# Kernel tuning notes

Hardware: AMD Instinct MI355X
Metric: run time of the kernel (lower is better)

## Reference

```python
import jax, jax.numpy as jnp
import numpy as np

N = 4096       # number of graph nodes
F_IN = 512     # in_features == out_features (residual connection requires it)
H = 8          # n_heads


def setup_inputs() -> dict:
    key = jax.random.key(0)
    k1, k2, k3, k4, k5 = jax.random.split(key, 5)
    s = 1.0 / np.sqrt(F_IN)  # keep projections well-scaled
    x = jax.random.normal(k1, (N, F_IN), dtype=jnp.float32)
    Wq = jax.random.normal(k2, (F_IN, F_IN), dtype=jnp.float32) * s
    Wk = jax.random.normal(k3, (F_IN, F_IN), dtype=jnp.float32) * s
    Wv = jax.random.normal(k4, (F_IN, F_IN), dtype=jnp.float32) * s
    adj = jax.random.randint(k5, (H, N, N), 0, 2, dtype=jnp.int32)
    return {"x": x, "Wq": Wq, "Wk": Wk, "Wv": Wv, "adj": adj}


def reference(x, Wq, Wk, Wv, adj):
    # Faithful to torch GraphAttentionLayer.forward (eval mode, dropout off).
    # NOTE: the torch code builds keys = input.repeat(N,1,1).detach() -> the
    # K/V inputs are stop-gradient copies of x; projections are per-node, so
    # we compute them once instead of materializing the redundant [N,N,F].
    n, f = x.shape
    d = f // H  # head dim (chunk_size)
    xk = jax.lax.stop_gradient(x)
    # nn.Linear: y = x @ W.T ; split feature dim into heads -> [H, N, d]
    Q = (x @ Wq.T).reshape(n, H, d).transpose(1, 0, 2)
    K = (xk @ Wk.T).reshape(n, H, d).transpose(1, 0, 2)
    V = (xk @ Wv.T).reshape(n, H, d).transpose(1, 0, 2)
    # scaled by sqrt(in_features) (NOT head dim), as in the original
    scores = jnp.einsum('hnd,hmd->hnm', Q, K) / jnp.sqrt(jnp.float32(f))
    scores = jnp.where(adj > 0, scores, jnp.float32(-9e15))
    attn = jax.nn.softmax(scores, axis=-1)          # [H, N, N]
    out = jnp.einsum('hnm,hmd->hnd', attn, V)       # [H, N, d]
    out = out.transpose(1, 0, 2).reshape(n, f)      # concat heads -> [N, F]
    return jax.nn.elu(out + x)[:, None, :]          # [N, 1, F] like torch
```

## Files before the change

### kernel.cpp

```cpp
#include <hip/hip_runtime.h>
#include <hip/hip_bf16.h>

#define NN 4096
#define FF 512
#define NH 8
#define DH 64

typedef __attribute__((ext_vector_type(8))) short bf16x8;
typedef __attribute__((ext_vector_type(4))) float f32x4;

#define X_OFF  0
#define W_OFF  2097152
#define QF_OFF 2883584
#define KF_OFF 4980736
#define VF_OFF 7077888
#define PACC_OFF 9175040
#define PDEN_USHORT_OFF 25952256

__device__ __forceinline__ ushort f2bf(float f) {
    __hip_bfloat16 h = __float2bfloat16(f);
    return __builtin_bit_cast(ushort, h);
}
__device__ __forceinline__ float bf2f(ushort u) {
    unsigned int v = ((unsigned int)u) << 16;
    return __builtin_bit_cast(float, v);
}

__global__ __launch_bounds__(256) void cvt_kernel(const float* __restrict__ x,
                                                  const float* __restrict__ wq,
                                                  const float* __restrict__ wk,
                                                  const float* __restrict__ wv,
                                                  ushort* __restrict__ ws) {
    int i = blockIdx.x * 256 + threadIdx.x;
    int base = i * 4;
    const float* src;
    int off;
    float sc = 1.f;
    if (base < 2097152) { src = x; off = base; }
    else {
        int t = base - 2097152;
        int m = t >> 18;
        src = (m == 0) ? wq : ((m == 1) ? wk : wv);
        if (m == 0) sc = 0.044194173824159216f;
        off = t & 262143;
    }
    float4 v = *reinterpret_cast<const float4*>(src + off);
    ushort4 o;
    o.x = f2bf(v.x * sc); o.y = f2bf(v.y * sc); o.z = f2bf(v.z * sc); o.w = f2bf(v.w * sc);
    *reinterpret_cast<ushort4*>(ws + base) = o;
}

__global__ __launch_bounds__(256) void qkv_kernel(ushort* __restrict__ ws) {
    int bx = blockIdx.x;
    int mat = bx >> 3;
    int fb  = bx & 7;
    int mb  = blockIdx.y;
    int wave = threadIdx.x >> 6, lane = threadIdx.x & 63;
    int la = lane & 15, lk = lane >> 4;

    int m_base = mb * 64 + wave * 16;
    int f_base = fb * 64;

    const ushort* xb = ws + X_OFF;
    const ushort* wb = ws + W_OFF + mat * 262144;

    f32x4 acc[4];
#pragma unroll
    for (int t = 0; t < 4; ++t) acc[t] = (f32x4){0.f, 0.f, 0.f, 0.f};

#pragma unroll 4
    for (int k0 = 0; k0 < 512; k0 += 32) {
        bf16x8 a = *reinterpret_cast<const bf16x8*>(xb + (size_t)(m_base + la) * 512 + k0 + lk * 8);
#pragma unroll
        for (int ft = 0; ft < 4; ++ft) {
            bf16x8 b = *reinterpret_cast<const bf16x8*>(wb + (size_t)(f_base + ft * 16 + la) * 512 + k0 + lk * 8);
            acc[ft] = __builtin_amdgcn_mfma_f32_16x16x32_bf16(a, b, acc[ft], 0, 0, 0);
        }
    }

#pragma unroll
    for (int ft = 0; ft < 4; ++ft) {
#pragma unroll
        for (int r = 0; r < 4; ++r) {
            int n = m_base + lk * 4 + r;
            int d = ft * 16 + la;
            ushort v = f2bf(acc[ft][r]);
            if (mat < 2) {
                ushort* base = ws + (mat == 0 ? QF_OFF : KF_OFF) + (size_t)fb * 262144;
                int blk = n >> 4, rr = n & 15;
                int half = d >> 5, lkk = (d >> 3) & 3, e = d & 7;
                base[(((size_t)blk * 2 + half) * 64 + lkk * 16 + rr) * 8 + e] = v;
            } else {
                ushort* base = ws + VF_OFF + (size_t)fb * 262144;
                int kb64 = n >> 6, kc = n & 63;
                int hf = kc >> 5, lkv = (kc >> 3) & 3, ev = kc & 7;
                int dt = d >> 4, lav = d & 15;
                base[((((size_t)kb64 * 4 + dt) * 2 + hf) * 64 + lkv * 16 + lav) * 8 + ev] = v;
            }
        }
    }
}


#define STAGE(BUF, KB)                                                                     \
    {                                                                                      \
        const ushort* sbase_ = (wave < 2) ? Kh : Vh;                                       \
        ushort(*dbuf_)[512] = (wave < 2) ? kbuf[BUF] : vbuf[BUF];                          \
        int t0_ = (wave & 1) * 4;                                                          \
        _Pragma("unroll")                                                                  \
        for (int t_ = 0; t_ < 4; ++t_) {                                                   \
            int tile_ = t0_ + t_;                                                          \
            const ushort* src_ = sbase_ +                                                  \
                (((size_t)(KB) * 4 + (tile_ >> 1)) * 2 + (tile_ & 1)) * 512 + lane * 8;    \
            __builtin_amdgcn_global_load_lds(                                              \
                (const __attribute__((address_space(1))) unsigned int*)src_,               \
                (__attribute__((address_space(3))) unsigned int*)&dbuf_[tile_][0],         \
                16, 0, 0);                                                                 \
        }                                                                                  \
    }

__global__ __launch_bounds__(256, 3) void attn_kernel(const int* __restrict__ adj,
                                                      const ushort* __restrict__ ws,
                                                      ushort* __restrict__ pacc,
                                                      float* __restrict__ pden) {
    __shared__ ushort kbuf[2][8][512];
    __shared__ ushort vbuf[2][8][512];
    __shared__ ushort P[4][16][72];

    int bid = blockIdx.x;
    int h = bid & 7, qb = (bid >> 3) & 63, ks = bid >> 9;
    int wave = threadIdx.x >> 6, lane = threadIdx.x & 63;
    int la = lane & 15, lk = lane >> 4;
    int q0w = qb * 64 + wave * 16;

    const ushort* Qh = ws + QF_OFF + (size_t)h * 262144;
    const ushort* Kh = ws + KF_OFF + (size_t)h * 262144;
    const ushort* Vh = ws + VF_OFF + (size_t)h * 262144;
    const int* adjw = adj + (size_t)h * 16777216 + (size_t)q0w * 4096;

    bf16x8 qa0 = *reinterpret_cast<const bf16x8*>(Qh + ((((size_t)(q0w >> 4)) * 2 + 0) * 64 + lane) * 8);
    bf16x8 qa1 = *reinterpret_cast<const bf16x8*>(Qh + ((((size_t)(q0w >> 4)) * 2 + 1) * 64 + lane) * 8);

    f32x4 acc[4];
    float den[4];
#pragma unroll
    for (int r = 0; r < 4; ++r) {
        acc[r] = (f32x4){0.f, 0.f, 0.f, 0.f};
        den[r] = 0.f;
    }

    const f32x4 zero = {0.f, 0.f, 0.f, 0.f};
    int kbase = ks * 8;

    int adjv[16];
    STAGE(0, kbase)
    __builtin_amdgcn_sched_barrier(0);
#pragma unroll
    for (int kt = 0; kt < 4; ++kt)
#pragma unroll
        for (int r = 0; r < 4; ++r)
            adjv[kt * 4 + r] = __builtin_nontemporal_load(
                adjw + (size_t)(lk * 4 + r) * 4096 + (size_t)kbase * 64 + kt * 16 + la);
    __builtin_amdgcn_sched_barrier(0);

    for (int it = 0; it < 8; ++it) {
        int kb = kbase + it;
        int cur = it & 1;

        asm volatile("s_waitcnt vmcnt(16)" ::: "memory");
        __builtin_amdgcn_s_barrier();
        __builtin_amdgcn_sched_barrier(0);

#pragma unroll
        for (int kt = 0; kt < 4; ++kt) {
            bf16x8 kf0 = *reinterpret_cast<const bf16x8*>(&kbuf[cur][kt * 2 + 0][lane * 8]);
            bf16x8 kf1 = *reinterpret_cast<const bf16x8*>(&kbuf[cur][kt * 2 + 1][lane * 8]);
            f32x4 s = __builtin_amdgcn_mfma_f32_16x16x32_bf16(qa0, kf0, zero, 0, 0, 0);
            s = __builtin_amdgcn_mfma_f32_16x16x32_bf16(qa1, kf1, s, 0, 0, 0);
#pragma unroll
            for (int r = 0; r < 4; ++r) {
                float sv = adjv[kt * 4 + r] ? s[r] : -1e30f;
                float e = __expf(sv);
                den[r] += e;
                P[wave][lk * 4 + r][kt * 16 + la] = f2bf(e);
            }
        }

        bf16x8 pa0 = *reinterpret_cast<const bf16x8*>(&P[wave][la][lk * 8]);
        bf16x8 pa1 = *reinterpret_cast<const bf16x8*>(&P[wave][la][32 + lk * 8]);
#pragma unroll
        for (int dt = 0; dt < 4; ++dt) {
            bf16x8 vb0 = *reinterpret_cast<const bf16x8*>(&vbuf[cur][dt * 2 + 0][lane * 8]);
            bf16x8 vb1 = *reinterpret_cast<const bf16x8*>(&vbuf[cur][dt * 2 + 1][lane * 8]);
            acc[dt] = __builtin_amdgcn_mfma_f32_16x16x32_bf16(pa0, vb0, acc[dt], 0, 0, 0);
            acc[dt] = __builtin_amdgcn_mfma_f32_16x16x32_bf16(pa1, vb1, acc[dt], 0, 0, 0);
        }

        if (it < 7) {
            __builtin_amdgcn_sched_barrier(0);
            STAGE(cur ^ 1, kb + 1)
            __builtin_amdgcn_sched_barrier(0);
#pragma unroll
            for (int kt = 0; kt < 4; ++kt)
#pragma unroll
                for (int r = 0; r < 4; ++r)
                    adjv[kt * 4 + r] = __builtin_nontemporal_load(
                        adjw + (size_t)(lk * 4 + r) * 4096 + (size_t)(kb + 1) * 64 + kt * 16 + la);
            __builtin_amdgcn_sched_barrier(0);
        }
    }

#pragma unroll
    for (int r = 0; r < 4; ++r)
#pragma unroll
        for (int mm = 1; mm < 16; mm <<= 1)
            den[r] += __shfl_xor(den[r], mm, 64);

    ushort* pa_out = pacc + ((size_t)ks * 8 + h) * 4096 * 64;
#pragma unroll
    for (int dt = 0; dt < 4; ++dt)
#pragma unroll
        for (int r = 0; r < 4; ++r) {
            int q = q0w + lk * 4 + r;
            __builtin_nontemporal_store(f2bf(acc[dt][r]), pa_out + (size_t)q * 64 + dt * 16 + la);
        }
    if (la == 0) {
        float* pd = pden + ((size_t)ks * 8 + h) * 4096;
#pragma unroll
        for (int r = 0; r < 4; ++r)
            pd[q0w + lk * 4 + r] = den[r];
    }
}

__global__ __launch_bounds__(256) void combine_kernel(const float* __restrict__ x,
                                                      const ushort* __restrict__ pacc,
                                                      const float* __restrict__ pden,
                                                      float* __restrict__ out) {
    int idx = blockIdx.x * 256 + threadIdx.x;
    int n = idx >> 7, fq = idx & 127;
    int h = fq >> 4;
    int d4 = (fq & 15) * 4;

    float4 o = make_float4(0.f, 0.f, 0.f, 0.f);
    float den = 0.f;
#pragma unroll
    for (int ksp = 0; ksp < 8; ++ksp) {
        const ushort* pa = pacc + (((size_t)ksp * 8 + h) * 4096 + n) * 64 + d4;
        ushort4 p = *reinterpret_cast<const ushort4*>(pa);
        o.x += bf2f(p.x); o.y += bf2f(p.y); o.z += bf2f(p.z); o.w += bf2f(p.w);
        den += pden[((size_t)ksp * 8 + h) * 4096 + n];
    }
    float4 xv = *reinterpret_cast<const float4*>(x + (size_t)n * 512 + fq * 4);
    float inv = 1.f / den;
    float4 r;
    r.x = o.x * inv + xv.x;
    r.y = o.y * inv + xv.y;
    r.z = o.z * inv + xv.z;
    r.w = o.w * inv + xv.w;
    r.x = (r.x > 0.f) ? r.x : (__expf(r.x) - 1.f);
    r.y = (r.y > 0.f) ? r.y : (__expf(r.y) - 1.f);
    r.z = (r.z > 0.f) ? r.z : (__expf(r.z) - 1.f);
    r.w = (r.w > 0.f) ? r.w : (__expf(r.w) - 1.f);
    *reinterpret_cast<float4*>(out + (size_t)n * 512 + fq * 4) = r;
}

extern "C" void kernel_launch(void* const* d_in, const int* in_sizes, int n_in,
                              void* d_out, int out_size, void* d_ws, size_t ws_size,
                              hipStream_t stream) {
    const float* x  = (const float*)d_in[0];
    const float* wq = (const float*)d_in[1];
    const float* wk = (const float*)d_in[2];
    const float* wv = (const float*)d_in[3];
    const int*   adj = (const int*)d_in[4];
    float* out = (float*)d_out;
    ushort* ws = (ushort*)d_ws;
    ushort* pacc = ws + PACC_OFF;
    float* pden = (float*)(ws + PDEN_USHORT_OFF);

    cvt_kernel<<<2816, 256, 0, stream>>>(x, wq, wk, wv, ws);
    qkv_kernel<<<dim3(24, 64), 256, 0, stream>>>(ws);
    attn_kernel<<<4096, 256, 0, stream>>>(adj, ws, pacc, pden);
    combine_kernel<<<2048, 256, 0, stream>>>(x, pacc, pden, out);
}
```

Baseline: 226.6 us.

## Process two query sub-tiles per wave and prefetch next block before compute

Each wave now handles 32 query rows instead of 16, so every K/V tile staged in LDS is reused for twice the query rows and the grid halves to 2048 blocks. The adjacency values are packed into a 32-bit mask right after the wait, and the prefetch of the next K/V block and adjacency is issued before the current block's compute rather than after it, to hide load latency. The cost is more registers (32 adj ints, doubled accumulators), which may lower occupancy, and the wait is now vmcnt(0), a full drain.

```diff
diff --git a/kernel.cpp b/kernel.cpp
--- a/kernel.cpp
+++ b/kernel.cpp
@@ -119,116 +119,143 @@
         }                                                                                  \
     }
 
+#define ADJ_LOAD(KB)                                                                       \
+    {                                                                                      \
+        _Pragma("unroll")                                                                  \
+        for (int qs_ = 0; qs_ < 2; ++qs_)                                                  \
+            _Pragma("unroll")                                                              \
+            for (int kt_ = 0; kt_ < 4; ++kt_)                                              \
+                _Pragma("unroll")                                                          \
+                for (int r_ = 0; r_ < 4; ++r_)                                             \
+                    adjv[qs_ * 16 + kt_ * 4 + r_] = __builtin_nontemporal_load(            \
+                        adjw + (size_t)(qs_ * 16 + lk * 4 + r_) * 4096 +                   \
+                        (size_t)(KB) * 64 + kt_ * 16 + la);                                \
+    }
+
 __global__ __launch_bounds__(256, 3) void attn_kernel(const int* __restrict__ adj,
                                                       const ushort* __restrict__ ws,
                                                       ushort* __restrict__ pacc,
                                                       float* __restrict__ pden) {
     __shared__ ushort kbuf[2][8][512];
     __shared__ ushort vbuf[2][8][512];
-    __shared__ ushort P[4][16][72];
+    __shared__ ushort P[4][32][72];
 
     int bid = blockIdx.x;
-    int h = bid & 7, qb = (bid >> 3) & 63, ks = bid >> 9;
+    int h = bid & 7, qb = (bid >> 3) & 31, ks = bid >> 8;
     int wave = threadIdx.x >> 6, lane = threadIdx.x & 63;
     int la = lane & 15, lk = lane >> 4;
-    int q0w = qb * 64 + wave * 16;
+    int q0w = qb * 128 + wave * 32;
 
     const ushort* Qh = ws + QF_OFF + (size_t)h * 262144;
     const ushort* Kh = ws + KF_OFF + (size_t)h * 262144;
     const ushort* Vh = ws + VF_OFF + (size_t)h * 262144;
     const int* adjw = adj + (size_t)h * 16777216 + (size_t)q0w * 4096;
 
-    bf16x8 qa0 = *reinterpret_cast<const bf16x8*>(Qh + ((((size_t)(q0w >> 4)) * 2 + 0) * 64 + lane) * 8);
-    bf16x8 qa1 = *reinterpret_cast<const bf16x8*>(Qh + ((((size_t)(q0w >> 4)) * 2 + 1) * 64 + lane) * 8);
-
-    f32x4 acc[4];
-    float den[4];
-#pragma unroll
-    for (int r = 0; r < 4; ++r) {
-        acc[r] = (f32x4){0.f, 0.f, 0.f, 0.f};
-        den[r] = 0.f;
-    }
+    bf16x8 qa[2][2];
+#pragma unroll
+    for (int qs = 0; qs < 2; ++qs)
+#pragma unroll
+        for (int hf = 0; hf < 2; ++hf)
+            qa[qs][hf] = *reinterpret_cast<const bf16x8*>(
+                Qh + ((((size_t)((q0w >> 4) + qs)) * 2 + hf) * 64 + lane) * 8);
+
+    f32x4 acc[2][4];
+    float den[2][4];
+#pragma unroll
+    for (int qs = 0; qs < 2; ++qs)
+#pragma unroll
+        for (int r = 0; r < 4; ++r) {
+            acc[qs][r] = (f32x4){0.f, 0.f, 0.f, 0.f};
+            den[qs][r] = 0.f;
+        }
 
     const f32x4 zero = {0.f, 0.f, 0.f, 0.f};
     int kbase = ks * 8;
 
-    int adjv[16];
+    int adjv[32];
     STAGE(0, kbase)
     __builtin_amdgcn_sched_barrier(0);
-#pragma unroll
-    for (int kt = 0; kt < 4; ++kt)
-#pragma unroll
-        for (int r = 0; r < 4; ++r)
-            adjv[kt * 4 + r] = __builtin_nontemporal_load(
-                adjw + (size_t)(lk * 4 + r) * 4096 + (size_t)kbase * 64 + kt * 16 + la);
+    ADJ_LOAD(kbase)
     __builtin_amdgcn_sched_barrier(0);
 
     for (int it = 0; it < 8; ++it) {
         int kb = kbase + it;
         int cur = it & 1;
 
-        asm volatile("s_waitcnt vmcnt(16)" ::: "memory");
+        asm volatile("s_waitcnt vmcnt(0)" ::: "memory");
         __builtin_amdgcn_s_barrier();
+
+        unsigned int mbits = 0u;
+#pragma unroll
+        for (int j = 0; j < 32; ++j)
+            mbits |= (adjv[j] != 0 ? 1u : 0u) << j;
+        __builtin_amdgcn_sched_barrier(0);
+
+        if (it < 7) {
+            STAGE(cur ^ 1, kb + 1)
+            __builtin_amdgcn_sched_barrier(0);
+            ADJ_LOAD(kb + 1)
+        }
         __builtin_amdgcn_sched_barrier(0);
 
 #pragma unroll
         for (int kt = 0; kt < 4; ++kt) {
             bf16x8 kf0 = *reinterpret_cast<const bf16x8*>(&kbuf[cur][kt * 2 + 0][lane * 8]);
             bf16x8 kf1 = *reinterpret_cast<const bf16x8*>(&kbuf[cur][kt * 2 + 1][lane * 8]);
-            f32x4 s = __builtin_amdgcn_mfma_f32_16x16x32_bf16(qa0, kf0, zero, 0, 0, 0);
-            s = __builtin_amdgcn_mfma_f32_16x16x32_bf16(qa1, kf1, s, 0, 0, 0);
-#pragma unroll
-            for (int r = 0; r < 4; ++r) {
-                float sv = adjv[kt * 4 + r] ? s[r] : -1e30f;
-                float e = __expf(sv);
-                den[r] += e;
-                P[wave][lk * 4 + r][kt * 16 + la] = f2bf(e);
+#pragma unroll
+            for (int qs = 0; qs < 2; ++qs) {
+                f32x4 s = __builtin_amdgcn_mfma_f32_16x16x32_bf16(qa[qs][0], kf0, zero, 0, 0, 0);
+                s = __builtin_amdgcn_mfma_f32_16x16x32_bf16(qa[qs][1], kf1, s, 0, 0, 0);
+#pragma unroll
+                for (int r = 0; r < 4; ++r) {
+                    float sv = ((mbits >> (qs * 16 + kt * 4 + r)) & 1u) ? s[r] : -1e30f;
+                    float e = __expf(sv);
+                    den[qs][r] += e;
+                    P[wave][qs * 16 + lk * 4 + r][kt * 16 + la] = f2bf(e);
+                }
             }
         }
 
-        bf16x8 pa0 = *reinterpret_cast<const bf16x8*>(&P[wave][la][lk * 8]);
-        bf16x8 pa1 = *reinterpret_cast<const bf16x8*>(&P[wave][la][32 + lk * 8]);
+        bf16x8 pa0q0 = *reinterpret_cast<const bf16x8*>(&P[wave][la][lk * 8]);
+        bf16x8 pa1q0 = *reinterpret_cast<const bf16x8*>(&P[wave][la][32 + lk * 8]);
+        bf16x8 pa0q1 = *reinterpret_cast<const bf16x8*>(&P[wave][16 + la][lk * 8]);
+        bf16x8 pa1q1 = *reinterpret_cast<const bf16x8*>(&P[wave][16 + la][32 + lk * 8]);
 #pragma unroll
         for (int dt = 0; dt < 4; ++dt) {
             bf16x8 vb0 = *reinterpret_cast<const bf16x8*>(&vbuf[cur][dt * 2 + 0][lane * 8]);
             bf16x8 vb1 = *reinterpret_cast<const bf16x8*>(&vbuf[cur][dt * 2 + 1][lane * 8]);
-            acc[dt] = __builtin_amdgcn_mfma_f32_16x16x32_bf16(pa0, vb0, acc[dt], 0, 0, 0);
-            acc[dt] = __builtin_amdgcn_mfma_f32_16x16x32_bf16(pa1, vb1, acc[dt], 0, 0, 0);
-        }
-
-        if (it < 7) {
-            __builtin_amdgcn_sched_barrier(0);
-            STAGE(cur ^ 1, kb + 1)
-            __builtin_amdgcn_sched_barrier(0);
-#pragma unroll
-            for (int kt = 0; kt < 4; ++kt)
-#pragma unroll
-                for (int r = 0; r < 4; ++r)
-                    adjv[kt * 4 + r] = __builtin_nontemporal_load(
-                        adjw + (size_t)(lk * 4 + r) * 4096 + (size_t)(kb + 1) * 64 + kt * 16 + la);
-            __builtin_amdgcn_sched_barrier(0);
-        }
-    }
-
-#pragma unroll
-    for (int r = 0; r < 4; ++r)
-#pragma unroll
-        for (int mm = 1; mm < 16; mm <<= 1)
-            den[r] += __shfl_xor(den[r], mm, 64);
+            acc[0][dt] = __builtin_amdgcn_mfma_f32_16x16x32_bf16(pa0q0, vb0, acc[0][dt], 0, 0, 0);
+            acc[0][dt] = __builtin_amdgcn_mfma_f32_16x16x32_bf16(pa1q0, vb1, acc[0][dt], 0, 0, 0);
+            acc[1][dt] = __builtin_amdgcn_mfma_f32_16x16x32_bf16(pa0q1, vb0, acc[1][dt], 0, 0, 0);
+            acc[1][dt] = __builtin_amdgcn_mfma_f32_16x16x32_bf16(pa1q1, vb1, acc[1][dt], 0, 0, 0);
+        }
+    }
+
+#pragma unroll
+    for (int qs = 0; qs < 2; ++qs)
+#pragma unroll
+        for (int r = 0; r < 4; ++r)
+#pragma unroll
+            for (int mm = 1; mm < 16; mm <<= 1)
+                den[qs][r] += __shfl_xor(den[qs][r], mm, 64);
 
     ushort* pa_out = pacc + ((size_t)ks * 8 + h) * 4096 * 64;
 #pragma unroll
-    for (int dt = 0; dt < 4; ++dt)
-#pragma unroll
-        for (int r = 0; r < 4; ++r) {
-            int q = q0w + lk * 4 + r;
-            __builtin_nontemporal_store(f2bf(acc[dt][r]), pa_out + (size_t)q * 64 + dt * 16 + la);
-        }
+    for (int qs = 0; qs < 2; ++qs)
+#pragma unroll
+        for (int dt = 0; dt < 4; ++dt)
+#pragma unroll
+            for (int r = 0; r < 4; ++r) {
+                int q = q0w + qs * 16 + lk * 4 + r;
+                __builtin_nontemporal_store(f2bf(acc[qs][dt][r]), pa_out + (size_t)q * 64 + dt * 16 + la);
+            }
     if (la == 0) {
         float* pd = pden + ((size_t)ks * 8 + h) * 4096;
 #pragma unroll
-        for (int r = 0; r < 4; ++r)
-            pd[q0w + lk * 4 + r] = den[r];
+        for (int qs = 0; qs < 2; ++qs)
+#pragma unroll
+            for (int r = 0; r < 4; ++r)
+                pd[q0w + qs * 16 + lk * 4 + r] = den[qs][r];
     }
 }
 
@@ -279,6 +306,6 @@
 
     cvt_kernel<<<2816, 256, 0, stream>>>(x, wq, wk, wv, ws);
     qkv_kernel<<<dim3(24, 64), 256, 0, stream>>>(ws);
-    attn_kernel<<<4096, 256, 0, stream>>>(adj, ws, pacc, pden);
+    attn_kernel<<<2048, 256, 0, stream>>>(adj, ws, pacc, pden);
     combine_kernel<<<2048, 256, 0, stream>>>(x, pacc, pden, out);
 }
```

Result: faster. 208.8 us (-7.8%).
